# Kernel optimization log

Hardware: AMD Instinct MI355X
Metric: run time of the kernel (lower is better)

Reference implementation:

```python
import jax, jax.numpy as jnp
import numpy as np

N = 500000
H = 256
HET = 3
AH = 128
B = 64


def setup_inputs() -> dict:
    key = jax.random.key(0)
    ks = jax.random.split(key, 6)
    x = jax.random.normal(ks[0], (N, H), dtype=jnp.float32)
    het = jax.random.uniform(ks[1], (N, HET), dtype=jnp.float32)
    batch = jnp.sort(jax.random.randint(ks[2], (N,), 0, B)).astype(jnp.int64)
    # xavier-uniform linear weights (stored already transposed: [in, out])
    def xavier(k, fan_in, fan_out):
        bound = np.sqrt(6.0 / (fan_in + fan_out))
        return jax.random.uniform(k, (fan_in, fan_out), dtype=jnp.float32,
                                  minval=-bound, maxval=bound)
    W1 = xavier(ks[3], H + HET, AH)
    b1 = jnp.zeros((AH,), dtype=jnp.float32)
    W2 = xavier(ks[4], AH, 1)
    b2 = jnp.zeros((1,), dtype=jnp.float32)
    Wv = xavier(ks[5], H, H)
    bv = jnp.zeros((H,), dtype=jnp.float32)
    return {"x": x, "het": het, "batch": batch,
            "W1": W1, "b1": b1, "W2": W2, "b2": b2, "Wv": Wv, "bv": bv}


def reference(x, het, batch, W1, b1, W2, b2, Wv, bv):
    # gate MLP: Linear -> tanh -> Linear, on [h_i ; het_i]
    gate_in = jnp.concatenate([x, het], axis=-1)              # [N, H+HET]
    raw = jnp.tanh(gate_in @ W1 + b1) @ W2 + b2               # [N, 1]
    # per-graph (segment) softmax over nodes
    seg_max = jax.ops.segment_max(raw, batch, num_segments=B)  # [B, 1]
    seg_max = jnp.where(jnp.isfinite(seg_max), seg_max, 0.0)   # empty segments
    e = jnp.exp(raw - seg_max[batch])                          # [N, 1]
    denom = jax.ops.segment_sum(e, batch, num_segments=B)      # [B, 1]
    attn = e / denom[batch]                                    # [N, 1]
    # weighted scatter-sum of projected values
    values = x @ Wv + bv                                       # [N, H]
    z = jax.ops.segment_sum(attn * values, batch, num_segments=B)  # [B, H]
    return z, attn
```

## Files before the change

kernel.cpp:

```cpp
#include <hip/hip_runtime.h>
#include <hip/hip_fp16.h>

#define H 256
#define HETD 3
#define AH 128
#define BSEG 64

typedef _Float16 half8 __attribute__((ext_vector_type(8)));
typedef __attribute__((ext_vector_type(4))) float f32x4;

__global__ void pack_w1_kernel(const float* __restrict__ W1,
                               unsigned short* __restrict__ W1p) {
    int idx = blockIdx.x * 256 + threadIdx.x;
    if (idx >= 9 * 8 * 64 * 8) return;
    int j    = idx & 7;
    int lane = (idx >> 3) & 63;
    int nt   = (idx >> 9) & 7;
    int t    = idx >> 12;
    int n = nt * 16 + (lane & 15);
    int k = t * 32 + ((lane >> 4) & 3) * 8 + j;
    float w = (k < (H + HETD)) ? W1[k * AH + n] : 0.f;
    __half hw = __float2half(w);
    W1p[idx] = __half_as_ushort(hw);
}

__device__ __forceinline__ _Float16 f2h(float f) { return (_Float16)f; }

__global__ __launch_bounds__(256) void gate_kernel(
    const float* __restrict__ x, const float* __restrict__ het,
    const int* __restrict__ batch, const unsigned short* __restrict__ W1p,
    const float* __restrict__ b1, const float* __restrict__ W2,
    const float* __restrict__ b2, float* __restrict__ p,
    float* __restrict__ d, int n_nodes)
{
    __shared__ float sW2[AH];
    __shared__ float sb1[AH];
    __shared__ float sd[BSEG];
    int tid = threadIdx.x;
    if (tid < AH) { sW2[tid] = W2[tid]; sb1[tid] = b1[tid]; }
    if (tid < BSEG) sd[tid] = 0.f;
    __syncthreads();

    int lane = tid & 63;
    int wv   = tid >> 6;
    int row  = lane & 15;
    int quad = lane >> 4;
    long long base = ((long long)blockIdx.x * 4 + wv) * 64;

    if (base < n_nodes) {
        f32x4 acc[4][8] = {};
        int nodeA[4];
#pragma unroll
        for (int m = 0; m < 4; ++m) {
            long long nd = base + m * 16 + row;
            nodeA[m] = (int)(nd < n_nodes ? nd : (long long)(n_nodes - 1));
        }
        const uint4* W1p4 = (const uint4*)W1p;

        for (int t = 0; t < 8; ++t) {
            half8 a[4];
#pragma unroll
            for (int m = 0; m < 4; ++m) {
                const float4* xr =
                    (const float4*)(x + (size_t)nodeA[m] * H + t * 32 + quad * 8);
                float4 lo = xr[0];
                float4 hi = xr[1];
                half8 av;
                av[0] = f2h(lo.x); av[1] = f2h(lo.y);
                av[2] = f2h(lo.z); av[3] = f2h(lo.w);
                av[4] = f2h(hi.x); av[5] = f2h(hi.y);
                av[6] = f2h(hi.z); av[7] = f2h(hi.w);
                a[m] = av;
            }
#pragma unroll
            for (int nt = 0; nt < 8; ++nt) {
                union { uint4 u; half8 h; } cv;
                cv.u = W1p4[(t * 8 + nt) * 64 + lane];
#pragma unroll
                for (int m = 0; m < 4; ++m)
                    acc[m][nt] = __builtin_amdgcn_mfma_f32_16x16x32_f16(
                        a[m], cv.h, acc[m][nt], 0, 0, 0);
            }
        }
        {
            half8 a[4];
#pragma unroll
            for (int m = 0; m < 4; ++m) {
                half8 av = {0, 0, 0, 0, 0, 0, 0, 0};
                if (quad == 0) {
                    const float* hr = het + (size_t)nodeA[m] * HETD;
                    av[0] = f2h(hr[0]); av[1] = f2h(hr[1]); av[2] = f2h(hr[2]);
                }
                a[m] = av;
            }
#pragma unroll
            for (int nt = 0; nt < 8; ++nt) {
                union { uint4 u; half8 h; } cv;
                cv.u = W1p4[(8 * 8 + nt) * 64 + lane];
#pragma unroll
                for (int m = 0; m < 4; ++m)
                    acc[m][nt] = __builtin_amdgcn_mfma_f32_16x16x32_f16(
                        a[m], cv.h, acc[m][nt], 0, 0, 0);
            }
        }

        float b2v = b2[0];
#pragma unroll
        for (int m = 0; m < 4; ++m) {
#pragma unroll
            for (int r = 0; r < 4; ++r) {
                float partial = 0.f;
#pragma unroll
                for (int nt = 0; nt < 8; ++nt) {
                    int n = nt * 16 + row;
                    float h = acc[m][nt][r] + sb1[n];
                    float e2 = __expf(2.f * h);
                    partial += (1.f - 2.f / (e2 + 1.f)) * sW2[n];
                }
                partial += __shfl_xor(partial, 1);
                partial += __shfl_xor(partial, 2);
                partial += __shfl_xor(partial, 4);
                partial += __shfl_xor(partial, 8);
                long long node = base + m * 16 + quad * 4 + r;
                if (row == r && node < n_nodes) {
                    float pe = __expf(partial + b2v);
                    p[node] = pe;
                    atomicAdd(&sd[batch[node]], pe);
                }
            }
        }
    }
    __syncthreads();
    if (tid < BSEG) {
        float v = sd[tid];
        if (v != 0.f) atomicAdd(&d[tid], v);
    }
}

__global__ __launch_bounds__(256) void accum_kernel(
    const float* __restrict__ x, const float* __restrict__ p,
    const int* __restrict__ batch, float* __restrict__ S, int n_nodes)
{
    const int TILE = 512;
    int tid = threadIdx.x;
    int c4 = tid & 63;
    int ng = tid >> 6;
    long long start = (long long)blockIdx.x * TILE;
    long long end = start + TILE;
    if (end > n_nodes) end = n_nodes;
    if (start >= n_nodes) return;

    float ax = 0.f, ay = 0.f, az = 0.f, aw = 0.f;
    int cur = -1;
    for (long long i = start + ng; i < end; i += 4) {
        int sg = batch[i];
        float pi = p[i];
        if (sg != cur) {
            if (cur >= 0) {
                float* Sp = S + cur * H + c4 * 4;
                atomicAdd(Sp + 0, ax); atomicAdd(Sp + 1, ay);
                atomicAdd(Sp + 2, az); atomicAdd(Sp + 3, aw);
            }
            cur = sg; ax = ay = az = aw = 0.f;
        }
        float4 xv = ((const float4*)(x + (size_t)i * H))[c4];
        ax += pi * xv.x; ay += pi * xv.y; az += pi * xv.z; aw += pi * xv.w;
    }
    if (cur >= 0) {
        float* Sp = S + cur * H + c4 * 4;
        atomicAdd(Sp + 0, ax); atomicAdd(Sp + 1, ay);
        atomicAdd(Sp + 2, az); atomicAdd(Sp + 3, aw);
    }
}

__global__ void attn_kernel(const float* __restrict__ p,
                            const int* __restrict__ batch,
                            const float* __restrict__ d,
                            float* __restrict__ attn, int n_nodes) {
    int i = blockIdx.x * 256 + threadIdx.x;
    if (i < n_nodes) attn[i] = p[i] / d[batch[i]];
}

__global__ __launch_bounds__(256) void z_kernel(
    const float* __restrict__ S, const float* __restrict__ d,
    const float* __restrict__ Wv, const float* __restrict__ bv,
    float* __restrict__ z)
{
    __shared__ float sA[H];
    int b = blockIdx.x;
    int j = threadIdx.x;
    float dv = d[b];
    float inv = (dv != 0.f) ? 1.f / dv : 0.f;
    sA[j] = S[b * H + j] * inv;
    __syncthreads();
    float sum = (dv != 0.f) ? bv[j] : 0.f;
#pragma unroll 4
    for (int h = 0; h < H; ++h)
        sum += sA[h] * Wv[h * H + j];
    z[b * H + j] = sum;
}

extern "C" void kernel_launch(void* const* d_in, const int* in_sizes, int n_in,
                              void* d_out, int out_size, void* d_ws, size_t ws_size,
                              hipStream_t stream)
{
    const float* x   = (const float*)d_in[0];
    const float* het = (const float*)d_in[1];
    const int*   bat = (const int*)d_in[2];
    const float* W1  = (const float*)d_in[3];
    const float* b1  = (const float*)d_in[4];
    const float* W2  = (const float*)d_in[5];
    const float* b2  = (const float*)d_in[6];
    const float* Wv  = (const float*)d_in[7];
    const float* bv  = (const float*)d_in[8];
    int n = in_sizes[0] / H;

    float* wsf = (float*)d_ws;
    float* d_d = wsf;
    float* d_S = wsf + BSEG;
    float* d_p = wsf + BSEG + BSEG * H;
    unsigned short* d_W1p = (unsigned short*)(wsf + BSEG + BSEG * H + n);

    hipMemsetAsync(d_d, 0, (BSEG + BSEG * H) * sizeof(float), stream);
    pack_w1_kernel<<<(9 * 8 * 64 * 8 + 255) / 256, 256, 0, stream>>>(W1, d_W1p);

    int waves = (n + 63) / 64;
    gate_kernel<<<(waves + 3) / 4, 256, 0, stream>>>(x, het, bat, d_W1p,
                                                     b1, W2, b2, d_p, d_d, n);
    accum_kernel<<<(n + 511) / 512, 256, 0, stream>>>(x, d_p, bat, d_S, n);
    attn_kernel<<<(n + 255) / 256, 256, 0, stream>>>(d_p, bat, d_d,
                                                     (float*)d_out + BSEG * H, n);
    z_kernel<<<BSEG, 256, 0, stream>>>(d_S, d_d, Wv, bv, (float*)d_out);
}
```

Baseline: 885.9 us.

## Fuse gate MLP and weighted accumulation, staging x as fp16 in LDS

Merges the gate kernel and the accumulation kernel so each block stages its 128 node rows of x as fp16 in shared memory and reuses them for the weighted segment sum. This removes the second full pass over x in global memory. In exchange it uses large LDS per block, which lowers occupancy, and halves the m-tiles per wave, which reduces W1 reuse. It also multiplies the number of global atomics into S and accumulates from fp16-rounded x.

```diff
diff --git a/kernel.cpp b/kernel.cpp
--- a/kernel.cpp
+++ b/kernel.cpp
@@ -5,8 +5,11 @@
 #define HETD 3
 #define AH 128
 #define BSEG 64
+#define NB 128
+#define XPITCH 264
 
 typedef _Float16 half8 __attribute__((ext_vector_type(8)));
+typedef _Float16 half4 __attribute__((ext_vector_type(4)));
 typedef __attribute__((ext_vector_type(4))) float f32x4;
 
 __global__ void pack_w1_kernel(const float* __restrict__ W1,
@@ -26,41 +29,52 @@
 
 __device__ __forceinline__ _Float16 f2h(float f) { return (_Float16)f; }
 
-__global__ __launch_bounds__(256) void gate_kernel(
+__global__ __launch_bounds__(256) void fused_gate_accum(
     const float* __restrict__ x, const float* __restrict__ het,
     const int* __restrict__ batch, const unsigned short* __restrict__ W1p,
     const float* __restrict__ b1, const float* __restrict__ W2,
     const float* __restrict__ b2, float* __restrict__ p,
-    float* __restrict__ d, int n_nodes)
+    float* __restrict__ d, float* __restrict__ S, int n_nodes)
 {
+    __shared__ _Float16 sx[NB * XPITCH];
     __shared__ float sW2[AH];
     __shared__ float sb1[AH];
+    __shared__ float sp[NB];
+    __shared__ int   sbat[NB];
     __shared__ float sd[BSEG];
+
     int tid = threadIdx.x;
+    long long base = (long long)blockIdx.x * NB;
+
     if (tid < AH) { sW2[tid] = W2[tid]; sb1[tid] = b1[tid]; }
     if (tid < BSEG) sd[tid] = 0.f;
+    if (tid < NB) {
+        sp[tid] = 0.f;
+        long long nd = base + tid;
+        sbat[tid] = batch[nd < n_nodes ? nd : (long long)(n_nodes - 1)];
+    }
     __syncthreads();
 
     int lane = tid & 63;
     int wv   = tid >> 6;
     int row  = lane & 15;
     int quad = lane >> 4;
-    long long base = ((long long)blockIdx.x * 4 + wv) * 64;
-
-    if (base < n_nodes) {
-        f32x4 acc[4][8] = {};
-        int nodeA[4];
-#pragma unroll
-        for (int m = 0; m < 4; ++m) {
-            long long nd = base + m * 16 + row;
+    long long wbase = base + (long long)wv * 32;
+
+    if (wbase < n_nodes) {
+        f32x4 acc[2][8] = {};
+        int nodeA[2];
+#pragma unroll
+        for (int m = 0; m < 2; ++m) {
+            long long nd = wbase + m * 16 + row;
             nodeA[m] = (int)(nd < n_nodes ? nd : (long long)(n_nodes - 1));
         }
         const uint4* W1p4 = (const uint4*)W1p;
 
         for (int t = 0; t < 8; ++t) {
-            half8 a[4];
-#pragma unroll
-            for (int m = 0; m < 4; ++m) {
+            half8 a[2];
+#pragma unroll
+            for (int m = 0; m < 2; ++m) {
                 const float4* xr =
                     (const float4*)(x + (size_t)nodeA[m] * H + t * 32 + quad * 8);
                 float4 lo = xr[0];
@@ -71,21 +85,23 @@
                 av[4] = f2h(hi.x); av[5] = f2h(hi.y);
                 av[6] = f2h(hi.z); av[7] = f2h(hi.w);
                 a[m] = av;
+                *(half8*)&sx[(wv * 32 + m * 16 + row) * XPITCH
+                             + t * 32 + quad * 8] = av;
             }
 #pragma unroll
             for (int nt = 0; nt < 8; ++nt) {
                 union { uint4 u; half8 h; } cv;
                 cv.u = W1p4[(t * 8 + nt) * 64 + lane];
 #pragma unroll
-                for (int m = 0; m < 4; ++m)
+                for (int m = 0; m < 2; ++m)
                     acc[m][nt] = __builtin_amdgcn_mfma_f32_16x16x32_f16(
                         a[m], cv.h, acc[m][nt], 0, 0, 0);
             }
         }
         {
-            half8 a[4];
-#pragma unroll
-            for (int m = 0; m < 4; ++m) {
+            half8 a[2];
+#pragma unroll
+            for (int m = 0; m < 2; ++m) {
                 half8 av = {0, 0, 0, 0, 0, 0, 0, 0};
                 if (quad == 0) {
                     const float* hr = het + (size_t)nodeA[m] * HETD;
@@ -98,7 +114,7 @@
                 union { uint4 u; half8 h; } cv;
                 cv.u = W1p4[(8 * 8 + nt) * 64 + lane];
 #pragma unroll
-                for (int m = 0; m < 4; ++m)
+                for (int m = 0; m < 2; ++m)
                     acc[m][nt] = __builtin_amdgcn_mfma_f32_16x16x32_f16(
                         a[m], cv.h, acc[m][nt], 0, 0, 0);
             }
@@ -106,70 +122,65 @@
 
         float b2v = b2[0];
 #pragma unroll
-        for (int m = 0; m < 4; ++m) {
+        for (int m = 0; m < 2; ++m) {
 #pragma unroll
             for (int r = 0; r < 4; ++r) {
                 float partial = 0.f;
 #pragma unroll
                 for (int nt = 0; nt < 8; ++nt) {
-                    int n = nt * 16 + row;
-                    float h = acc[m][nt][r] + sb1[n];
+                    int nn = nt * 16 + row;
+                    float h = acc[m][nt][r] + sb1[nn];
                     float e2 = __expf(2.f * h);
-                    partial += (1.f - 2.f / (e2 + 1.f)) * sW2[n];
+                    partial += (1.f - 2.f / (e2 + 1.f)) * sW2[nn];
                 }
                 partial += __shfl_xor(partial, 1);
                 partial += __shfl_xor(partial, 2);
                 partial += __shfl_xor(partial, 4);
                 partial += __shfl_xor(partial, 8);
-                long long node = base + m * 16 + quad * 4 + r;
+                int nl = wv * 32 + m * 16 + quad * 4 + r;
+                long long node = base + nl;
                 if (row == r && node < n_nodes) {
                     float pe = __expf(partial + b2v);
                     p[node] = pe;
-                    atomicAdd(&sd[batch[node]], pe);
+                    sp[nl] = pe;
+                    atomicAdd(&sd[sbat[nl]], pe);
                 }
             }
         }
     }
     __syncthreads();
+
     if (tid < BSEG) {
         float v = sd[tid];
         if (v != 0.f) atomicAdd(&d[tid], v);
     }
-}
-
-__global__ __launch_bounds__(256) void accum_kernel(
-    const float* __restrict__ x, const float* __restrict__ p,
-    const int* __restrict__ batch, float* __restrict__ S, int n_nodes)
-{
-    const int TILE = 512;
-    int tid = threadIdx.x;
-    int c4 = tid & 63;
-    int ng = tid >> 6;
-    long long start = (long long)blockIdx.x * TILE;
-    long long end = start + TILE;
-    if (end > n_nodes) end = n_nodes;
-    if (start >= n_nodes) return;
-
-    float ax = 0.f, ay = 0.f, az = 0.f, aw = 0.f;
-    int cur = -1;
-    for (long long i = start + ng; i < end; i += 4) {
-        int sg = batch[i];
-        float pi = p[i];
-        if (sg != cur) {
-            if (cur >= 0) {
-                float* Sp = S + cur * H + c4 * 4;
-                atomicAdd(Sp + 0, ax); atomicAdd(Sp + 1, ay);
-                atomicAdd(Sp + 2, az); atomicAdd(Sp + 3, aw);
-            }
-            cur = sg; ax = ay = az = aw = 0.f;
-        }
-        float4 xv = ((const float4*)(x + (size_t)i * H))[c4];
-        ax += pi * xv.x; ay += pi * xv.y; az += pi * xv.z; aw += pi * xv.w;
-    }
-    if (cur >= 0) {
-        float* Sp = S + cur * H + c4 * 4;
-        atomicAdd(Sp + 0, ax); atomicAdd(Sp + 1, ay);
-        atomicAdd(Sp + 2, az); atomicAdd(Sp + 3, aw);
+
+    {
+        float a0 = 0.f, a1 = 0.f, a2 = 0.f, a3 = 0.f;
+        int cur = -1;
+        for (int i = wv; i < NB; i += 4) {
+            if (base + i >= n_nodes) break;
+            int sg = sbat[i];
+            float pi = sp[i];
+            if (sg != cur) {
+                if (cur >= 0) {
+                    float* Sp = S + cur * H + lane * 4;
+                    atomicAdd(Sp + 0, a0); atomicAdd(Sp + 1, a1);
+                    atomicAdd(Sp + 2, a2); atomicAdd(Sp + 3, a3);
+                }
+                cur = sg; a0 = a1 = a2 = a3 = 0.f;
+            }
+            half4 xv = *(const half4*)&sx[i * XPITCH + lane * 4];
+            a0 += pi * (float)xv[0];
+            a1 += pi * (float)xv[1];
+            a2 += pi * (float)xv[2];
+            a3 += pi * (float)xv[3];
+        }
+        if (cur >= 0) {
+            float* Sp = S + cur * H + lane * 4;
+            atomicAdd(Sp + 0, a0); atomicAdd(Sp + 1, a1);
+            atomicAdd(Sp + 2, a2); atomicAdd(Sp + 3, a3);
+        }
     }
 }
 
@@ -224,10 +235,9 @@
     hipMemsetAsync(d_d, 0, (BSEG + BSEG * H) * sizeof(float), stream);
     pack_w1_kernel<<<(9 * 8 * 64 * 8 + 255) / 256, 256, 0, stream>>>(W1, d_W1p);
 
-    int waves = (n + 63) / 64;
-    gate_kernel<<<(waves + 3) / 4, 256, 0, stream>>>(x, het, bat, d_W1p,
-                                                     b1, W2, b2, d_p, d_d, n);
-    accum_kernel<<<(n + 511) / 512, 256, 0, stream>>>(x, d_p, bat, d_S, n);
+    int blocks = (n + NB - 1) / NB;
+    fused_gate_accum<<<blocks, 256, 0, stream>>>(x, het, bat, d_W1p, b1, W2, b2,
+                                                 d_p, d_d, d_S, n);
     attn_kernel<<<(n + 255) / 256, 256, 0, stream>>>(d_p, bat, d_d,
                                                      (float*)d_out + BSEG * H, n);
     z_kernel<<<BSEG, 256, 0, stream>>>(d_S, d_d, Wv, bv, (float*)d_out);
```

New measurement: 977.0 us. 10.3% more time.
